# Performance work log

Measured on AMD Instinct MI355X. Metric: run time of the kernel, lower is better.

## Reference

```python
import jax, jax.numpy as jnp
import numpy as np

B = 2048
PARAM_SHAPES = {
    'l1c0': (1, 8, 3, 3), 'l1c1': (3, 4, 8, 2), 'l1c2': (2, 4, 8, 2), 'l1c3': (2, 4, 8, 2), 'l1c4': (2, 4, 8, 1), 'b1': (8, 4, 4, 4, 4),
    'l2c0': (1, 4, 8, 2), 'l2c1': (2, 2, 4, 2), 'l2c2': (2, 2, 4, 2), 'l2c3': (2, 2, 4, 2), 'l2c4': (2, 2, 4, 1), 'b2': (4, 2, 2, 2, 2),
    'l3c0': (1, 2, 4, 2), 'l3c1': (2, 2, 2, 2), 'l3c2': (2, 2, 2, 2), 'l3c3': (2, 2, 2, 2), 'l3c4': (2, 2, 2, 1), 'b3': (2, 2, 2, 2, 2),
    'W': (2, 32), 'bl': (2,),
}

def setup_inputs():
    key = jax.random.key(0)
    ks = jax.random.split(key, len(PARAM_SHAPES) + 1)
    inp = {'x': jax.random.normal(ks[0], (B, 3, 8, 8, 8, 8), dtype=jnp.float32)}
    for k, (name, shp) in zip(ks[1:], PARAM_SHAPES.items()):
        scale = 0.5 if name[0] == 'l' and name != 'bl' else 0.1
        inp[name] = jax.random.normal(k, shp, dtype=jnp.float32) * scale
    return inp

def tt_linear(x, cores, bias):
    # y[b, m1..md] = sum_{n1..nd} W[m1..md, n1..nd] x[b, n1..nd] + bias[m1..md]
    # W is the TT-matrix with cores G_k of shape (r_{k-1}, m_k, n_k, r_k).
    b = x.shape[0]
    z = x.reshape(b, 1, -1)  # (B, rank, flat=[n_k..n_d, m_1..m_{k-1}])
    for G in cores:
        r0, m, n, r1 = G.shape
        z = jnp.einsum('brns,rmnq->bqsm', z.reshape(b, r0, n, -1), G).reshape(b, r1, -1)
    return z.reshape((b,) + bias.shape) + bias

def reference(x, l1c0, l1c1, l1c2, l1c3, l1c4, b1, l2c0, l2c1, l2c2, l2c3, l2c4, b2, l3c0, l3c1, l3c2, l3c3, l3c4, b3, W, bl):
    h = jax.nn.relu(tt_linear(x, [l1c0, l1c1, l1c2, l1c3, l1c4], b1))
    h = jax.nn.relu(tt_linear(h, [l2c0, l2c1, l2c2, l2c3, l2c4], b2))
    h = jax.nn.relu(tt_linear(h, [l3c0, l3c1, l3c2, l3c3, l3c4], b3))
    logits = h.reshape(-1, 32) @ W.T + bl  # (B, 2)
    return jax.nn.log_softmax(logits, axis=1)
```

## Files before the change

kernel.cpp:

```cpp
#include <hip/hip_runtime.h>
#include <math.h>

#define WC3  0
#define WC2  128
#define WU1  256
#define T2S  288
#define T3S  1440
#define H1O  288
#define AO   2528
#define BO   288
#define CO   1440
#define DO   1984
#define H2O  2256
#define H3O  2320
#define LDS_FLOATS 4576

__global__ void tt_setup_w3(const float* __restrict__ v0, const float* __restrict__ v1,
                            const float* __restrict__ v2, const float* __restrict__ v3,
                            const float* __restrict__ v4, float* __restrict__ w3) {
    int i = blockIdx.x * 256 + threadIdx.x;
    if (i >= 2048) return;
    int mi = i >> 6, nj = i & 63;
    int m1 = (mi >> 4) & 1, m2 = (mi >> 3) & 1, m3 = (mi >> 2) & 1, m4 = (mi >> 1) & 1, m5 = mi & 1;
    int n1 = (nj >> 4) & 3, n2 = (nj >> 3) & 1, n3 = (nj >> 2) & 1, n4 = (nj >> 1) & 1, n5 = nj & 1;
    float s = 0.f;
#pragma unroll
    for (int q1 = 0; q1 < 2; ++q1) {
        float a1 = v0[(m1 * 4 + n1) * 2 + q1];
#pragma unroll
        for (int q2 = 0; q2 < 2; ++q2) {
            float a2 = a1 * v1[((q1 * 2 + m2) * 2 + n2) * 2 + q2];
#pragma unroll
            for (int q3 = 0; q3 < 2; ++q3) {
                float a3 = a2 * v2[((q2 * 2 + m3) * 2 + n3) * 2 + q3];
#pragma unroll
                for (int q4 = 0; q4 < 2; ++q4)
                    s = fmaf(a3 * v3[((q3 * 2 + m4) * 2 + n4) * 2 + q4],
                             v4[(q4 * 2 + m5) * 2 + n5], s);
            }
        }
    }
    w3[i] = s;
}

__global__ __launch_bounds__(64, 2)
void tt_main(const float* __restrict__ x,
             const float* __restrict__ g0, const float* __restrict__ g1,
             const float* __restrict__ g2, const float* __restrict__ g3,
             const float* __restrict__ g4, const float* __restrict__ b1g,
             const float* __restrict__ u0, const float* __restrict__ u1,
             const float* __restrict__ u2, const float* __restrict__ u3,
             const float* __restrict__ u4, const float* __restrict__ b2g,
             const float* __restrict__ b3g,
             const float* __restrict__ Wmg, const float* __restrict__ blg,
             const float* __restrict__ w3g,
             float* __restrict__ out)
{
    __shared__ float smem[LDS_FLOATS];
    const int t = threadIdx.x;
    const int b = blockIdx.x;
    const float* xb = x + (size_t)b * 12288;

    float xv[32];
    {
        const float4* xq = (const float4*)xb + t * 8;
#pragma unroll
        for (int i = 0; i < 8; ++i) {
            const float4 v = xq[i];
            xv[i*4+0] = v.x; xv[i*4+1] = v.y; xv[i*4+2] = v.z; xv[i*4+3] = v.w;
        }
    }

    smem[WC3 + t] = g3[t];  smem[WC3 + 64 + t] = g3[64 + t];
    smem[WC2 + t] = g2[t];  smem[WC2 + 64 + t] = g2[64 + t];
    if (t < 32) smem[WU1 + t] = u1[t];
    __syncthreads();

    const int h = t & 1;
    const int p = t >> 1;

    float regT4[36];
#pragma unroll
    for (int i = 0; i < 36; ++i) regT4[i] = 0.f;

#pragma unroll
    for (int n1 = 0; n1 < 3; ++n1) {
#pragma unroll
        for (int n2h = 0; n2h < 2; ++n2h) {
            const int s = n1 * 2 + n2h;
            float xn[32];
            if (s < 5) {
                const float4* xq = (const float4*)xb + (s + 1) * 512 + t * 8;
#pragma unroll
                for (int i = 0; i < 8; ++i) {
                    const float4 v = xq[i];
                    xn[i*4+0] = v.x; xn[i*4+1] = v.y; xn[i*4+2] = v.z; xn[i*4+3] = v.w;
                }
            }

            float t1[32];
#pragma unroll
            for (int m5 = 0; m5 < 4; ++m5)
#pragma unroll
            for (int q4 = 0; q4 < 2; ++q4) {
                const float* w = g4 + (q4 * 4 + m5) * 8;
#pragma unroll
                for (int n4l = 0; n4l < 4; ++n4l) {
                    float sa = xv[n4l*8+0] * w[0];
#pragma unroll
                    for (int n5 = 1; n5 < 8; ++n5) sa = fmaf(xv[n4l*8+n5], w[n5], sa);
                    t1[n4l*8 + m5*2 + q4] = sa;
                }
            }

            float acc[16];
#pragma unroll
            for (int i = 0; i < 16; ++i) acc[i] = 0.f;
#pragma unroll
            for (int pass = 0; pass < 2; ++pass) {
                const int hh = (pass == 0) ? h : (1 - h);
                if (pass == 1) {
#pragma unroll
                    for (int i = 0; i < 32; ++i) t1[i] = __shfl_xor(t1[i], 1);
                }
#pragma unroll
                for (int m4 = 0; m4 < 4; ++m4) {
                    const int cbase = WC3 + ((h * 4 + m4) * 8 + hh * 4) * 2;
                    const float4 c0 = *(const float4*)&smem[cbase];
                    const float4 c1 = *(const float4*)&smem[cbase + 4];
                    const float cs[8] = {c0.x, c0.y, c0.z, c0.w, c1.x, c1.y, c1.z, c1.w};
#pragma unroll
                    for (int m5 = 0; m5 < 4; ++m5) {
                        float sa = acc[m4*4+m5];
#pragma unroll
                        for (int n4l = 0; n4l < 4; ++n4l)
#pragma unroll
                        for (int q4 = 0; q4 < 2; ++q4)
                            sa = fmaf(t1[n4l*8 + m5*2 + q4], cs[n4l*2 + q4], sa);
                        acc[m4*4+m5] = sa;
                    }
                }
            }

            __syncthreads();
#pragma unroll
            for (int m45 = 0; m45 < 16; ++m45)
                smem[T2S + p * 36 + m45 * 2 + h] = acc[m45];
            __syncthreads();

            {
                const int n3h = t & 1;
                const int q2  = (t >> 1) & 1;
                const int m3  = (t >> 2) & 3;
                const int n2l = t >> 4;
                float o3[16];
#pragma unroll
                for (int i = 0; i < 16; ++i) o3[i] = 0.f;
#pragma unroll
                for (int n3l = 0; n3l < 4; ++n3l) {
                    const int rb = T2S + (n2l * 8 + n3h * 4 + n3l) * 36;
                    float rv[32];
#pragma unroll
                    for (int g = 0; g < 8; ++g) {
                        const float4 v = *(const float4*)&smem[rb + g * 4];
                        rv[g*4+0] = v.x; rv[g*4+1] = v.y; rv[g*4+2] = v.z; rv[g*4+3] = v.w;
                    }
                    const int wb = WC2 + ((q2 * 4 + m3) * 8 + n3h * 4 + n3l) * 2;
                    const float w0 = smem[wb], w1 = smem[wb + 1];
#pragma unroll
                    for (int m45 = 0; m45 < 16; ++m45)
                        o3[m45] = fmaf(rv[m45*2], w0, fmaf(rv[m45*2+1], w1, o3[m45]));
                }
#pragma unroll
                for (int k = 0; k < 16; ++k) o3[k] += __shfl_xor(o3[k], 1);
                const int row = n2h * 16 + n2l * 4 + m3;
#pragma unroll
                for (int k = 0; k < 8; ++k) {
                    const float v = n3h ? o3[8 + k] : o3[k];
                    smem[T3S + row * 34 + (n3h * 8 + k) * 2 + q2] = v;
                }
            }
            if (s < 5) {
#pragma unroll
                for (int i = 0; i < 32; ++i) xv[i] = xn[i];
            }
        }
        __syncthreads();

        {
            const int m3 = t >> 4, m4 = (t >> 2) & 3, m5 = t & 3;
            float2 zz[8];
#pragma unroll
            for (int n2 = 0; n2 < 8; ++n2)
                zz[n2] = *(const float2*)&smem[T3S + (n2 * 4 + m3) * 34 + (m4 * 4 + m5) * 2];
#pragma unroll
            for (int jj = 0; jj < 4; ++jj)
#pragma unroll
            for (int q1 = 0; q1 < 3; ++q1) {
                float sa = regT4[jj * 9 + n1 * 3 + q1];
#pragma unroll
                for (int n2g = 0; n2g < 4; ++n2g) {
                    const float4 w = *(const float4*)(g1 + ((q1 * 4 + jj) * 8 + n2g * 2) * 2);
                    sa = fmaf(zz[n2g*2].x,   w.x, sa);
                    sa = fmaf(zz[n2g*2].y,   w.y, sa);
                    sa = fmaf(zz[n2g*2+1].x, w.z, sa);
                    sa = fmaf(zz[n2g*2+1].y, w.w, sa);
                }
                regT4[jj * 9 + n1 * 3 + q1] = sa;
            }
        }
    }
    __syncthreads();

#pragma unroll
    for (int jj = 0; jj < 4; ++jj) {
        float bia[8];
#pragma unroll
        for (int m1 = 0; m1 < 8; ++m1) bia[m1] = b1g[m1 * 256 + jj * 64 + t];
#pragma unroll
        for (int m1 = 0; m1 < 8; ++m1) {
            float sa = bia[m1];
#pragma unroll
            for (int n1 = 0; n1 < 3; ++n1)
#pragma unroll
            for (int q1 = 0; q1 < 3; ++q1)
                sa = fmaf(regT4[jj * 9 + n1 * 3 + q1], g0[(m1 * 3 + n1) * 3 + q1], sa);
            smem[H1O + m1 * 256 + jj * 64 + t] = fmaxf(sa, 0.f);
        }
    }
    __syncthreads();

#pragma unroll
    for (int pp = 0; pp < 8; ++pp) {
        const int P = pp * 64 + t;
        const float4 hv = *(const float4*)&smem[H1O + P * 4];
        float4 av;
        av.x = hv.x*u4[0]  + hv.y*u4[1]  + hv.z*u4[2]  + hv.w*u4[3];
        av.y = hv.x*u4[8]  + hv.y*u4[9]  + hv.z*u4[10] + hv.w*u4[11];
        av.z = hv.x*u4[4]  + hv.y*u4[5]  + hv.z*u4[6]  + hv.w*u4[7];
        av.w = hv.x*u4[12] + hv.y*u4[13] + hv.z*u4[14] + hv.w*u4[15];
        *(float4*)&smem[AO + P * 4] = av;
    }
    __syncthreads();

#pragma unroll
    for (int pp = 0; pp < 2; ++pp) {
        const int p3 = pp * 64 + t;
        float4 aa[4];
#pragma unroll
        for (int n4 = 0; n4 < 4; ++n4)
            aa[n4] = *(const float4*)&smem[AO + (p3 * 4 + n4) * 4];
        float o[8];
#pragma unroll
        for (int i = 0; i < 8; ++i) o[i] = 0.f;
#pragma unroll
        for (int n4 = 0; n4 < 4; ++n4)
#pragma unroll
        for (int q4 = 0; q4 < 2; ++q4) {
            const float a0 = q4 ? aa[n4].y : aa[n4].x;
            const float a1 = q4 ? aa[n4].w : aa[n4].z;
#pragma unroll
            for (int q3 = 0; q3 < 2; ++q3)
#pragma unroll
            for (int m4 = 0; m4 < 2; ++m4) {
                const float w = u3[((q3 * 2 + m4) * 4 + n4) * 2 + q4];
                o[(m4 * 2 + 0) * 2 + q3] = fmaf(a0, w, o[(m4 * 2 + 0) * 2 + q3]);
                o[(m4 * 2 + 1) * 2 + q3] = fmaf(a1, w, o[(m4 * 2 + 1) * 2 + q3]);
            }
        }
#pragma unroll
        for (int k = 0; k < 8; ++k) smem[BO + p3 * 9 + k] = o[k];
    }
    __syncthreads();

    if (t < 32) {
        float o[16];
#pragma unroll
        for (int i = 0; i < 16; ++i) o[i] = 0.f;
#pragma unroll
        for (int n3 = 0; n3 < 4; ++n3)
#pragma unroll
        for (int q3 = 0; q3 < 2; ++q3) {
            float zb[4];
#pragma unroll
            for (int m45 = 0; m45 < 4; ++m45)
                zb[m45] = smem[BO + (t * 4 + n3) * 9 + m45 * 2 + q3];
#pragma unroll
            for (int m3 = 0; m3 < 2; ++m3)
#pragma unroll
            for (int q2 = 0; q2 < 2; ++q2) {
                const float w = u2[((q2 * 2 + m3) * 4 + n3) * 2 + q3];
#pragma unroll
                for (int m45 = 0; m45 < 4; ++m45)
                    o[(m3 * 4 + m45) * 2 + q2] = fmaf(zb[m45], w, o[(m3 * 4 + m45) * 2 + q2]);
            }
        }
#pragma unroll
        for (int k = 0; k < 16; ++k) smem[CO + t * 17 + k] = o[k];
    }
    __syncthreads();

    if (t < 32) {
        const int n1 = t >> 2, m2 = (t >> 1) & 1, m3 = t & 1;
        float o[8];
#pragma unroll
        for (int i = 0; i < 8; ++i) o[i] = 0.f;
#pragma unroll
        for (int n2 = 0; n2 < 4; ++n2)
#pragma unroll
        for (int q2 = 0; q2 < 2; ++q2) {
            float cb[4];
#pragma unroll
            for (int m45 = 0; m45 < 4; ++m45)
                cb[m45] = smem[CO + (n1 * 4 + n2) * 17 + (m3 * 4 + m45) * 2 + q2];
#pragma unroll
            for (int q1 = 0; q1 < 2; ++q1) {
                const float w = smem[WU1 + ((q1 * 2 + m2) * 4 + n2) * 2 + q2];
#pragma unroll
                for (int m45 = 0; m45 < 4; ++m45)
                    o[m45 * 2 + q1] = fmaf(cb[m45], w, o[m45 * 2 + q1]);
            }
        }
#pragma unroll
        for (int m45 = 0; m45 < 4; ++m45)
#pragma unroll
        for (int q1 = 0; q1 < 2; ++q1)
            smem[DO + (m2 * 8 + m3 * 4 + m45) * 17 + n1 * 2 + q1] = o[m45 * 2 + q1];
    }
    __syncthreads();

    if (t < 16) {
        float o[4];
#pragma unroll
        for (int i = 0; i < 4; ++i) o[i] = 0.f;
#pragma unroll
        for (int n1 = 0; n1 < 8; ++n1)
#pragma unroll
        for (int q1 = 0; q1 < 2; ++q1) {
            const float dv = smem[DO + t * 17 + n1 * 2 + q1];
#pragma unroll
            for (int m1 = 0; m1 < 4; ++m1)
                o[m1] = fmaf(dv, u0[(m1 * 8 + n1) * 2 + q1], o[m1]);
        }
#pragma unroll
        for (int m1 = 0; m1 < 4; ++m1)
            smem[H2O + m1 * 16 + t] = fmaxf(o[m1] + b2g[m1 * 16 + t], 0.f);
    }
    __syncthreads();

    if (t < 32) {
        const float4* wr = (const float4*)(w3g + t * 64);
        float sa = b3g[t];
#pragma unroll
        for (int g = 0; g < 16; ++g) {
            const float4 w4 = wr[g];
            sa = fmaf(w4.x, smem[H2O + g*4 + 0],
                 fmaf(w4.y, smem[H2O + g*4 + 1],
                 fmaf(w4.z, smem[H2O + g*4 + 2],
                 fmaf(w4.w, smem[H2O + g*4 + 3], sa))));
        }
        smem[H3O + t] = fmaxf(sa, 0.f);
    }
    __syncthreads();

    {
        const int k = t & 31;
        float pr = smem[H3O + k] * Wmg[t];
#pragma unroll
        for (int d = 16; d >= 1; d >>= 1) pr += __shfl_xor(pr, d);
        const float l0 = __shfl(pr, 0) + blg[0];
        const float l1 = __shfl(pr, 32) + blg[1];
        if (t == 0) {
            const float mm = fmaxf(l0, l1);
            const float lse = mm + logf(expf(l0 - mm) + expf(l1 - mm));
            out[(size_t)b * 2 + 0] = l0 - lse;
            out[(size_t)b * 2 + 1] = l1 - lse;
        }
    }
}

extern "C" void kernel_launch(void* const* d_in, const int* in_sizes, int n_in,
                              void* d_out, int out_size, void* d_ws, size_t ws_size,
                              hipStream_t stream) {
    const float* x    = (const float*)d_in[0];
    const float* l1c0 = (const float*)d_in[1];
    const float* l1c1 = (const float*)d_in[2];
    const float* l1c2 = (const float*)d_in[3];
    const float* l1c3 = (const float*)d_in[4];
    const float* l1c4 = (const float*)d_in[5];
    const float* b1   = (const float*)d_in[6];
    const float* l2c0 = (const float*)d_in[7];
    const float* l2c1 = (const float*)d_in[8];
    const float* l2c2 = (const float*)d_in[9];
    const float* l2c3 = (const float*)d_in[10];
    const float* l2c4 = (const float*)d_in[11];
    const float* b2   = (const float*)d_in[12];
    const float* l3c0 = (const float*)d_in[13];
    const float* l3c1 = (const float*)d_in[14];
    const float* l3c2 = (const float*)d_in[15];
    const float* l3c3 = (const float*)d_in[16];
    const float* l3c4 = (const float*)d_in[17];
    const float* b3   = (const float*)d_in[18];
    const float* Wm   = (const float*)d_in[19];
    const float* bl   = (const float*)d_in[20];
    float* W3 = (float*)d_ws;

    tt_setup_w3<<<8, 256, 0, stream>>>(l3c0, l3c1, l3c2, l3c3, l3c4, W3);
    tt_main<<<2048, 64, 0, stream>>>(x, l1c0, l1c1, l1c2, l1c3, l1c4, b1,
                                     l2c0, l2c1, l2c2, l2c3, l2c4, b2, b3,
                                     Wm, bl, W3, (float*)d_out);
}
```

Before: 209.1 us.

## Split layer-1 work across two wavefronts per block and compact LDS

Blocks grow from one to two wavefronts, each handling one of the two n2 halves per n1 step, so the layer-1 stages run in parallel. The explicit next-slice x prefetch into registers is dropped, and each wave loads its own slice directly. Layer-2 stages are fused and use fewer, padded LDS buffers, cutting LDS from about 18KB to about 14.7KB. The aim is higher occupancy and shorter per-block latency, at the cost of more block-wide barriers shared by two waves and the loss of the register prefetch.

New measurement: 277.8 us. 1.33x slower.

```diff
diff --git a/kernel.cpp b/kernel.cpp
--- a/kernel.cpp
+++ b/kernel.cpp
@@ -4,16 +4,13 @@
 #define WC3  0
 #define WC2  128
 #define WU1  256
-#define T2S  288
-#define T3S  1440
-#define H1O  288
-#define AO   2528
-#define BO   288
-#define CO   1440
-#define DO   1984
-#define H2O  2256
-#define H3O  2320
-#define LDS_FLOATS 4576
+#define T2A  288
+#define T3S  2592
+#define HZ   288
+#define DZ32 32
+#define H3O  (HZ + 2112)
+#define H2O  (HZ + 2176)
+#define LDS_FLOATS 3680
 
 __global__ void tt_setup_w3(const float* __restrict__ v0, const float* __restrict__ v1,
                             const float* __restrict__ v2, const float* __restrict__ v3,
@@ -43,7 +40,7 @@
     w3[i] = s;
 }
 
-__global__ __launch_bounds__(64, 2)
+__global__ __launch_bounds__(128, 4)
 void tt_main(const float* __restrict__ x,
              const float* __restrict__ g0, const float* __restrict__ g1,
              const float* __restrict__ g2, const float* __restrict__ g3,
@@ -58,218 +55,198 @@
 {
     __shared__ float smem[LDS_FLOATS];
     const int t = threadIdx.x;
+    const int v = t >> 6;
+    const int l = t & 63;
     const int b = blockIdx.x;
     const float* xb = x + (size_t)b * 12288;
 
-    float xv[32];
-    {
-        const float4* xq = (const float4*)xb + t * 8;
-#pragma unroll
-        for (int i = 0; i < 8; ++i) {
-            const float4 v = xq[i];
-            xv[i*4+0] = v.x; xv[i*4+1] = v.y; xv[i*4+2] = v.z; xv[i*4+3] = v.w;
-        }
-    }
-
-    smem[WC3 + t] = g3[t];  smem[WC3 + 64 + t] = g3[64 + t];
-    smem[WC2 + t] = g2[t];  smem[WC2 + 64 + t] = g2[64 + t];
+    smem[WC3 + t] = g3[t];
+    smem[WC2 + t] = g2[t];
     if (t < 32) smem[WU1 + t] = u1[t];
     __syncthreads();
 
-    const int h = t & 1;
-    const int p = t >> 1;
-
-    float regT4[36];
-#pragma unroll
-    for (int i = 0; i < 36; ++i) regT4[i] = 0.f;
+    const int h = l & 1;
+    const int p = l >> 1;
+    const int rho = (p & 7) * 4 + (p >> 3);
+    const int T2W = T2A + v * 1152;
+
+    float regT4[18];
+#pragma unroll
+    for (int i = 0; i < 18; ++i) regT4[i] = 0.f;
 
 #pragma unroll
     for (int n1 = 0; n1 < 3; ++n1) {
-#pragma unroll
-        for (int n2h = 0; n2h < 2; ++n2h) {
-            const int s = n1 * 2 + n2h;
-            float xn[32];
-            if (s < 5) {
-                const float4* xq = (const float4*)xb + (s + 1) * 512 + t * 8;
-#pragma unroll
-                for (int i = 0; i < 8; ++i) {
-                    const float4 v = xq[i];
-                    xn[i*4+0] = v.x; xn[i*4+1] = v.y; xn[i*4+2] = v.z; xn[i*4+3] = v.w;
+        const int s = n1 * 2 + v;
+        float xv[32];
+        {
+            const float4* xq = (const float4*)(xb + s * 2048 + l * 32);
+#pragma unroll
+            for (int i = 0; i < 8; ++i) {
+                const float4 q = xq[i];
+                xv[i*4+0] = q.x; xv[i*4+1] = q.y; xv[i*4+2] = q.z; xv[i*4+3] = q.w;
+            }
+        }
+        float t1[32];
+#pragma unroll
+        for (int m5 = 0; m5 < 4; ++m5)
+#pragma unroll
+        for (int q4 = 0; q4 < 2; ++q4) {
+            const float* w = g4 + (q4 * 4 + m5) * 8;
+#pragma unroll
+            for (int n4l = 0; n4l < 4; ++n4l) {
+                float sa = xv[n4l*8+0] * w[0];
+#pragma unroll
+                for (int n5 = 1; n5 < 8; ++n5) sa = fmaf(xv[n4l*8+n5], w[n5], sa);
+                t1[n4l*8 + m5*2 + q4] = sa;
+            }
+        }
+        float acc[16];
+#pragma unroll
+        for (int i = 0; i < 16; ++i) acc[i] = 0.f;
+#pragma unroll
+        for (int pass = 0; pass < 2; ++pass) {
+            const int hh = (pass == 0) ? h : (1 - h);
+            if (pass == 1) {
+#pragma unroll
+                for (int i = 0; i < 32; ++i) t1[i] = __shfl_xor(t1[i], 1);
+            }
+#pragma unroll
+            for (int m4 = 0; m4 < 4; ++m4) {
+                const int cbase = WC3 + ((h * 4 + m4) * 8 + hh * 4) * 2;
+                const float4 c0 = *(const float4*)&smem[cbase];
+                const float4 c1 = *(const float4*)&smem[cbase + 4];
+                const float cs[8] = {c0.x, c0.y, c0.z, c0.w, c1.x, c1.y, c1.z, c1.w};
+#pragma unroll
+                for (int m5 = 0; m5 < 4; ++m5) {
+                    float sa = acc[m4*4+m5];
+#pragma unroll
+                    for (int n4l = 0; n4l < 4; ++n4l)
+#pragma unroll
+                    for (int q4 = 0; q4 < 2; ++q4)
+                        sa = fmaf(t1[n4l*8 + m5*2 + q4], cs[n4l*2 + q4], sa);
+                    acc[m4*4+m5] = sa;
                 }
             }
-
-            float t1[32];
-#pragma unroll
-            for (int m5 = 0; m5 < 4; ++m5)
-#pragma unroll
-            for (int q4 = 0; q4 < 2; ++q4) {
-                const float* w = g4 + (q4 * 4 + m5) * 8;
-#pragma unroll
-                for (int n4l = 0; n4l < 4; ++n4l) {
-                    float sa = xv[n4l*8+0] * w[0];
-#pragma unroll
-                    for (int n5 = 1; n5 < 8; ++n5) sa = fmaf(xv[n4l*8+n5], w[n5], sa);
-                    t1[n4l*8 + m5*2 + q4] = sa;
+        }
+#pragma unroll
+        for (int m45 = 0; m45 < 16; ++m45)
+            smem[T2W + rho * 36 + m45 * 2 + h] = acc[m45];
+        __syncthreads();
+
+        {
+            const int n3h = l & 1;
+            const int q2  = (l >> 1) & 1;
+            const int m3  = (l >> 2) & 3;
+            const int n2l = l >> 4;
+            float o3[16];
+#pragma unroll
+            for (int i = 0; i < 16; ++i) o3[i] = 0.f;
+#pragma unroll
+            for (int n3l = 0; n3l < 4; ++n3l) {
+                const int n3 = n3h * 4 + n3l;
+                const int rb = T2W + (n3 * 4 + n2l) * 36;
+                float rv[32];
+#pragma unroll
+                for (int g = 0; g < 8; ++g) {
+                    const float4 q = *(const float4*)&smem[rb + g * 4];
+                    rv[g*4+0] = q.x; rv[g*4+1] = q.y; rv[g*4+2] = q.z; rv[g*4+3] = q.w;
                 }
-            }
-
-            float acc[16];
-#pragma unroll
-            for (int i = 0; i < 16; ++i) acc[i] = 0.f;
-#pragma unroll
-            for (int pass = 0; pass < 2; ++pass) {
-                const int hh = (pass == 0) ? h : (1 - h);
-                if (pass == 1) {
-#pragma unroll
-                    for (int i = 0; i < 32; ++i) t1[i] = __shfl_xor(t1[i], 1);
-                }
-#pragma unroll
-                for (int m4 = 0; m4 < 4; ++m4) {
-                    const int cbase = WC3 + ((h * 4 + m4) * 8 + hh * 4) * 2;
-                    const float4 c0 = *(const float4*)&smem[cbase];
-                    const float4 c1 = *(const float4*)&smem[cbase + 4];
-                    const float cs[8] = {c0.x, c0.y, c0.z, c0.w, c1.x, c1.y, c1.z, c1.w};
-#pragma unroll
-                    for (int m5 = 0; m5 < 4; ++m5) {
-                        float sa = acc[m4*4+m5];
-#pragma unroll
-                        for (int n4l = 0; n4l < 4; ++n4l)
-#pragma unroll
-                        for (int q4 = 0; q4 < 2; ++q4)
-                            sa = fmaf(t1[n4l*8 + m5*2 + q4], cs[n4l*2 + q4], sa);
-                        acc[m4*4+m5] = sa;
-                    }
-                }
-            }
-
-            __syncthreads();
-#pragma unroll
-            for (int m45 = 0; m45 < 16; ++m45)
-                smem[T2S + p * 36 + m45 * 2 + h] = acc[m45];
-            __syncthreads();
-
-            {
-                const int n3h = t & 1;
-                const int q2  = (t >> 1) & 1;
-                const int m3  = (t >> 2) & 3;
-                const int n2l = t >> 4;
-                float o3[16];
-#pragma unroll
-                for (int i = 0; i < 16; ++i) o3[i] = 0.f;
-#pragma unroll
-                for (int n3l = 0; n3l < 4; ++n3l) {
-                    const int rb = T2S + (n2l * 8 + n3h * 4 + n3l) * 36;
-                    float rv[32];
-#pragma unroll
-                    for (int g = 0; g < 8; ++g) {
-                        const float4 v = *(const float4*)&smem[rb + g * 4];
-                        rv[g*4+0] = v.x; rv[g*4+1] = v.y; rv[g*4+2] = v.z; rv[g*4+3] = v.w;
-                    }
-                    const int wb = WC2 + ((q2 * 4 + m3) * 8 + n3h * 4 + n3l) * 2;
-                    const float w0 = smem[wb], w1 = smem[wb + 1];
-#pragma unroll
-                    for (int m45 = 0; m45 < 16; ++m45)
-                        o3[m45] = fmaf(rv[m45*2], w0, fmaf(rv[m45*2+1], w1, o3[m45]));
-                }
-#pragma unroll
-                for (int k = 0; k < 16; ++k) o3[k] += __shfl_xor(o3[k], 1);
-                const int row = n2h * 16 + n2l * 4 + m3;
-#pragma unroll
-                for (int k = 0; k < 8; ++k) {
-                    const float v = n3h ? o3[8 + k] : o3[k];
-                    smem[T3S + row * 34 + (n3h * 8 + k) * 2 + q2] = v;
-                }
-            }
-            if (s < 5) {
-#pragma unroll
-                for (int i = 0; i < 32; ++i) xv[i] = xn[i];
+                const int wb = WC2 + ((q2 * 4 + m3) * 8 + n3) * 2;
+                const float w0 = smem[wb], w1 = smem[wb + 1];
+#pragma unroll
+                for (int m45 = 0; m45 < 16; ++m45)
+                    o3[m45] = fmaf(rv[m45*2], w0, fmaf(rv[m45*2+1], w1, o3[m45]));
+            }
+#pragma unroll
+            for (int k = 0; k < 16; ++k) o3[k] += __shfl_xor(o3[k], 1);
+            const int row3 = (v * 4 + n2l) * 4 + m3;
+#pragma unroll
+            for (int k = 0; k < 8; ++k) {
+                const float val = n3h ? o3[8 + k] : o3[k];
+                smem[T3S + row3 * 34 + (n3h * 8 + k) * 2 + q2] = val;
             }
         }
         __syncthreads();
 
         {
-            const int m3 = t >> 4, m4 = (t >> 2) & 3, m5 = t & 3;
+            const int m3 = l >> 4, m4 = (l >> 2) & 3, m5 = l & 3;
             float2 zz[8];
 #pragma unroll
             for (int n2 = 0; n2 < 8; ++n2)
                 zz[n2] = *(const float2*)&smem[T3S + (n2 * 4 + m3) * 34 + (m4 * 4 + m5) * 2];
 #pragma unroll
-            for (int jj = 0; jj < 4; ++jj)
-#pragma unroll
-            for (int q1 = 0; q1 < 3; ++q1) {
-                float sa = regT4[jj * 9 + n1 * 3 + q1];
-#pragma unroll
-                for (int n2g = 0; n2g < 4; ++n2g) {
-                    const float4 w = *(const float4*)(g1 + ((q1 * 4 + jj) * 8 + n2g * 2) * 2);
-                    sa = fmaf(zz[n2g*2].x,   w.x, sa);
-                    sa = fmaf(zz[n2g*2].y,   w.y, sa);
-                    sa = fmaf(zz[n2g*2+1].x, w.z, sa);
-                    sa = fmaf(zz[n2g*2+1].y, w.w, sa);
+            for (int jjl = 0; jjl < 2; ++jjl) {
+                const int jj = v * 2 + jjl;
+#pragma unroll
+                for (int q1 = 0; q1 < 3; ++q1) {
+                    float sa = regT4[(jjl * 3 + n1) * 3 + q1];
+#pragma unroll
+                    for (int n2g = 0; n2g < 4; ++n2g) {
+                        const float4 w = *(const float4*)(g1 + ((q1 * 4 + jj) * 8 + n2g * 2) * 2);
+                        sa = fmaf(zz[n2g*2].x,   w.x, sa);
+                        sa = fmaf(zz[n2g*2].y,   w.y, sa);
+                        sa = fmaf(zz[n2g*2+1].x, w.z, sa);
+                        sa = fmaf(zz[n2g*2+1].y, w.w, sa);
+                    }
+                    regT4[(jjl * 3 + n1) * 3 + q1] = sa;
                 }
-                regT4[jj * 9 + n1 * 3 + q1] = sa;
-            }
-        }
-    }
-    __syncthreads();
-
-#pragma unroll
-    for (int jj = 0; jj < 4; ++jj) {
-        float bia[8];
-#pragma unroll
-        for (int m1 = 0; m1 < 8; ++m1) bia[m1] = b1g[m1 * 256 + jj * 64 + t];
+            }
+        }
+        __syncthreads();
+    }
+
+#pragma unroll
+    for (int jjl = 0; jjl < 2; ++jjl) {
+        const int jj = v * 2 + jjl;
 #pragma unroll
         for (int m1 = 0; m1 < 8; ++m1) {
-            float sa = bia[m1];
+            const int e = m1 * 256 + jj * 64 + l;
+            float sa = b1g[e];
 #pragma unroll
             for (int n1 = 0; n1 < 3; ++n1)
 #pragma unroll
             for (int q1 = 0; q1 < 3; ++q1)
-                sa = fmaf(regT4[jj * 9 + n1 * 3 + q1], g0[(m1 * 3 + n1) * 3 + q1], sa);
-            smem[H1O + m1 * 256 + jj * 64 + t] = fmaxf(sa, 0.f);
-        }
-    }
-    __syncthreads();
-
-#pragma unroll
-    for (int pp = 0; pp < 8; ++pp) {
-        const int P = pp * 64 + t;
-        const float4 hv = *(const float4*)&smem[H1O + P * 4];
-        float4 av;
-        av.x = hv.x*u4[0]  + hv.y*u4[1]  + hv.z*u4[2]  + hv.w*u4[3];
-        av.y = hv.x*u4[8]  + hv.y*u4[9]  + hv.z*u4[10] + hv.w*u4[11];
-        av.z = hv.x*u4[4]  + hv.y*u4[5]  + hv.z*u4[6]  + hv.w*u4[7];
-        av.w = hv.x*u4[12] + hv.y*u4[13] + hv.z*u4[14] + hv.w*u4[15];
-        *(float4*)&smem[AO + P * 4] = av;
-    }
-    __syncthreads();
-
-#pragma unroll
-    for (int pp = 0; pp < 2; ++pp) {
-        const int p3 = pp * 64 + t;
-        float4 aa[4];
-#pragma unroll
-        for (int n4 = 0; n4 < 4; ++n4)
-            aa[n4] = *(const float4*)&smem[AO + (p3 * 4 + n4) * 4];
+                sa = fmaf(regT4[(jjl * 3 + n1) * 3 + q1], g0[(m1 * 3 + n1) * 3 + q1], sa);
+            smem[HZ + (e >> 4) * 17 + (e & 15)] = fmaxf(sa, 0.f);
+        }
+    }
+    __syncthreads();
+
+    {
+        float hv[16];
+#pragma unroll
+        for (int k = 0; k < 16; ++k) hv[k] = smem[HZ + t * 17 + k];
         float o[8];
 #pragma unroll
         for (int i = 0; i < 8; ++i) o[i] = 0.f;
 #pragma unroll
-        for (int n4 = 0; n4 < 4; ++n4)
-#pragma unroll
-        for (int q4 = 0; q4 < 2; ++q4) {
-            const float a0 = q4 ? aa[n4].y : aa[n4].x;
-            const float a1 = q4 ? aa[n4].w : aa[n4].z;
-#pragma unroll
-            for (int q3 = 0; q3 < 2; ++q3)
-#pragma unroll
-            for (int m4 = 0; m4 < 2; ++m4) {
-                const float w = u3[((q3 * 2 + m4) * 4 + n4) * 2 + q4];
-                o[(m4 * 2 + 0) * 2 + q3] = fmaf(a0, w, o[(m4 * 2 + 0) * 2 + q3]);
-                o[(m4 * 2 + 1) * 2 + q3] = fmaf(a1, w, o[(m4 * 2 + 1) * 2 + q3]);
-            }
-        }
-#pragma unroll
-        for (int k = 0; k < 8; ++k) smem[BO + p3 * 9 + k] = o[k];
+        for (int n4 = 0; n4 < 4; ++n4) {
+            float a[4];
+#pragma unroll
+            for (int m5 = 0; m5 < 2; ++m5)
+#pragma unroll
+            for (int q4 = 0; q4 < 2; ++q4) {
+                float sa = hv[n4*4+0] * u4[(q4 * 2 + m5) * 4 + 0];
+#pragma unroll
+                for (int n5 = 1; n5 < 4; ++n5)
+                    sa = fmaf(hv[n4*4+n5], u4[(q4 * 2 + m5) * 4 + n5], sa);
+                a[m5 * 2 + q4] = sa;
+            }
+#pragma unroll
+            for (int q4 = 0; q4 < 2; ++q4) {
+                const float a0 = a[0 * 2 + q4], a1 = a[1 * 2 + q4];
+#pragma unroll
+                for (int q3 = 0; q3 < 2; ++q3)
+#pragma unroll
+                for (int m4 = 0; m4 < 2; ++m4) {
+                    const float w = u3[((q3 * 2 + m4) * 4 + n4) * 2 + q4];
+                    o[(m4 * 2 + 0) * 2 + q3] = fmaf(a0, w, o[(m4 * 2 + 0) * 2 + q3]);
+                    o[(m4 * 2 + 1) * 2 + q3] = fmaf(a1, w, o[(m4 * 2 + 1) * 2 + q3]);
+                }
+            }
+        }
+#pragma unroll
+        for (int k = 0; k < 8; ++k) smem[HZ + t * 17 + k] = o[k];
     }
     __syncthreads();
 
@@ -284,7 +261,7 @@
             float zb[4];
 #pragma unroll
             for (int m45 = 0; m45 < 4; ++m45)
-                zb[m45] = smem[BO + (t * 4 + n3) * 9 + m45 * 2 + q3];
+                zb[m45] = smem[HZ + (t * 4 + n3) * 17 + m45 * 2 + q3];
 #pragma unroll
             for (int m3 = 0; m3 < 2; ++m3)
 #pragma unroll
@@ -296,7 +273,7 @@
             }
         }
 #pragma unroll
-        for (int k = 0; k < 16; ++k) smem[CO + t * 17 + k] = o[k];
+        for (int k = 0; k < 16; ++k) smem[HZ + t * 68 + k] = o[k];
     }
     __syncthreads();
 
@@ -312,7 +289,7 @@
             float cb[4];
 #pragma unroll
             for (int m45 = 0; m45 < 4; ++m45)
-                cb[m45] = smem[CO + (n1 * 4 + n2) * 17 + (m3 * 4 + m45) * 2 + q2];
+                cb[m45] = smem[HZ + (n1 * 4 + n2) * 68 + (m3 * 4 + m45) * 2 + q2];
 #pragma unroll
             for (int q1 = 0; q1 < 2; ++q1) {
                 const float w = smem[WU1 + ((q1 * 2 + m2) * 4 + n2) * 2 + q2];
@@ -325,7 +302,7 @@
         for (int m45 = 0; m45 < 4; ++m45)
 #pragma unroll
         for (int q1 = 0; q1 < 2; ++q1)
-            smem[DO + (m2 * 8 + m3 * 4 + m45) * 17 + n1 * 2 + q1] = o[m45 * 2 + q1];
+            smem[HZ + (m2 * 8 + m3 * 4 + m45) * 136 + DZ32 + n1 * 2 + q1] = o[m45 * 2 + q1];
     }
     __syncthreads();
 
@@ -337,7 +314,7 @@
         for (int n1 = 0; n1 < 8; ++n1)
 #pragma unroll
         for (int q1 = 0; q1 < 2; ++q1) {
-            const float dv = smem[DO + t * 17 + n1 * 2 + q1];
+            const float dv = smem[HZ + t * 136 + DZ32 + n1 * 2 + q1];
 #pragma unroll
             for (int m1 = 0; m1 < 4; ++m1)
                 o[m1] = fmaf(dv, u0[(m1 * 8 + n1) * 2 + q1], o[m1]);
@@ -363,7 +340,7 @@
     }
     __syncthreads();
 
-    {
+    if (t < 64) {
         const int k = t & 31;
         float pr = smem[H3O + k] * Wmg[t];
 #pragma unroll
@@ -406,7 +383,7 @@
     float* W3 = (float*)d_ws;
 
     tt_setup_w3<<<8, 256, 0, stream>>>(l3c0, l3c1, l3c2, l3c3, l3c4, W3);
-    tt_main<<<2048, 64, 0, stream>>>(x, l1c0, l1c1, l1c2, l1c3, l1c4, b1,
-                                     l2c0, l2c1, l2c2, l2c3, l2c4, b2, b3,
-                                     Wm, bl, W3, (float*)d_out);
+    tt_main<<<2048, 128, 0, stream>>>(x, l1c0, l1c1, l1c2, l1c3, l1c4, b1,
+                                      l2c0, l2c1, l2c2, l2c3, l2c4, b2, b3,
+                                      Wm, bl, W3, (float*)d_out);
 }
```
